# Optimization experiments

Measured on AMD Instinct MI355X. Metric: run time of the kernel, lower is better.

Reference implementation:

```python
import jax, jax.numpy as jnp
import numpy as np

B, L, D, H = 2, 2048, 512, 8
HD = D // H
DIL, WIN, CAUSAL = 2, 256, True
HIDDEN = 4 * D
EPS = 1e-5


def _layer_norm(x, w, b):
    m = jnp.mean(x, axis=-1, keepdims=True)
    v = jnp.mean(jnp.square(x - m), axis=-1, keepdims=True)
    return (x - m) * jax.lax.rsqrt(v + EPS) * w + b


def setup_inputs() -> dict:
    key = jax.random.key(0)
    ks = jax.random.split(key, 6)
    sc = 0.02
    return {
        "x": jax.random.normal(ks[0], (B, L, D), jnp.float32),
        "norm1_w": jnp.ones((D,), jnp.float32),
        "norm1_b": jnp.zeros((D,), jnp.float32),
        "qkv_w": jax.random.normal(ks[1], (3 * D, D), jnp.float32) * sc,
        "qkv_b": jnp.zeros((3 * D,), jnp.float32),
        "out_w": jax.random.normal(ks[2], (D, D), jnp.float32) * sc,
        "out_b": jnp.zeros((D,), jnp.float32),
        "norm2_w": jnp.ones((D,), jnp.float32),
        "norm2_b": jnp.zeros((D,), jnp.float32),
        "ffn_w1": jax.random.normal(ks[3], (HIDDEN, D), jnp.float32) * sc,
        "ffn_b1": jnp.zeros((HIDDEN,), jnp.float32),
        "ffn_w2": jax.random.normal(ks[4], (D, HIDDEN), jnp.float32) * sc,
        "ffn_b2": jnp.zeros((D,), jnp.float32),
    }


def reference(x, norm1_w, norm1_b, qkv_w, qkv_b, out_w, out_b,
              norm2_w, norm2_b, ffn_w1, ffn_b1, ffn_w2, ffn_b2):
    # pre-norm attention block
    h = _layer_norm(x, norm1_w, norm1_b)                       # [B,L,D]
    qkv = h @ qkv_w.T + qkv_b                                  # [B,L,3D]
    q, k, v = jnp.split(qkv, 3, axis=-1)

    def heads(t):  # [B,L,D] -> [B,H,L,HD]
        return t.reshape(B, L, H, HD).transpose(0, 2, 1, 3)

    q, k, v = heads(q), heads(k), heads(v)

    # dilated / windowed / causal keep mask (True = attend)
    idx = jnp.arange(L)
    delta = idx[:, None] - idx[None, :]                        # [L,L]
    keep = (delta % DIL) == 0
    keep &= jnp.abs(delta) <= WIN
    if CAUSAL:
        keep &= delta >= 0

    scale = 1.0 / np.sqrt(HD)
    scores = jnp.einsum('bhqd,bhkd->bhqk', q, k) * scale       # [B,H,L,L]
    scores = jnp.where(keep, scores, jnp.finfo(scores.dtype).min)
    attn = jax.nn.softmax(scores, axis=-1)
    o = jnp.einsum('bhqk,bhkd->bhqd', attn, v)                 # [B,H,L,HD]
    o = o.transpose(0, 2, 1, 3).reshape(B, L, D)
    o = o @ out_w.T + out_b

    x = x + o                                                  # residual (dropout p=0)

    # pre-norm FFN block
    h2 = _layer_norm(x, norm2_w, norm2_b)
    f = jax.nn.gelu(h2 @ ffn_w1.T + ffn_b1, approximate=False)
    f = f @ ffn_w2.T + ffn_b2
    return x + f
```

## Files before the change

kernel.cpp:

```cpp
#include <hip/hip_runtime.h>
#include <stdint.h>

typedef float f32x4 __attribute__((ext_vector_type(4)));
typedef unsigned short u16x4 __attribute__((ext_vector_type(4)));
typedef unsigned short u16x8 __attribute__((ext_vector_type(8)));
typedef __bf16 bf16x8 __attribute__((ext_vector_type(8)));

__device__ __forceinline__ unsigned short f2bf(float f) {
  unsigned u = __float_as_uint(f);
  u += 0x7fffu + ((u >> 16) & 1u);
  return (unsigned short)(u >> 16);
}
__device__ __forceinline__ float bf2f(unsigned short h) {
  return __uint_as_float(((unsigned)h) << 16);
}
__device__ __forceinline__ f32x4 mfma16x16x32(u16x8 a, u16x8 b, f32x4 c) {
  return __builtin_amdgcn_mfma_f32_16x16x32_bf16(
      __builtin_bit_cast(bf16x8, a), __builtin_bit_cast(bf16x8, b), c, 0, 0, 0);
}
__device__ __forceinline__ void gload_lds16(const unsigned short* g, unsigned short* l) {
  __builtin_amdgcn_global_load_lds((__attribute__((address_space(1))) void*)(g),
                                   (__attribute__((address_space(3))) void*)(l), 16, 0, 0);
}
__device__ __forceinline__ int xcd_swz(int bid, int nb) {
  int cpx = nb >> 3;
  return (bid & 7) * cpx + (bid >> 3);
}
__device__ __forceinline__ float gelu_f(float v) {
  float z = 0.7978845608f * (v + 0.044715f * v * v * v);
  float t = __expf(-2.0f * z);
  return v * (1.0f / (1.0f + t));
}

__global__ __launch_bounds__(256)
void prep(const float* __restrict__ wq, unsigned short* __restrict__ dst,
          const float* __restrict__ x, const float* __restrict__ nw,
          const float* __restrict__ nb, unsigned short* __restrict__ hout,
          unsigned short* __restrict__ xbf) {
  if (blockIdx.x < 768) {
    int e = (blockIdx.x * 256 + threadIdx.x) << 2;
    f32x4 v = *(const f32x4*)(wq + e);
    u16x4 o;
    #pragma unroll
    for (int i = 0; i < 4; ++i) o[i] = f2bf(v[i]);
    *(u16x4*)(dst + e) = o;
  } else {
    const int row = ((blockIdx.x - 768) << 2) + (threadIdx.x >> 6);
    const int lane = threadIdx.x & 63;
    const float* xr = x + (size_t)row * 512 + (lane << 3);
    f32x4 v0 = *(const f32x4*)xr;
    f32x4 v1 = *(const f32x4*)(xr + 4);
    float s = 0.f, s2 = 0.f;
    #pragma unroll
    for (int i = 0; i < 4; ++i) { s += v0[i] + v1[i]; s2 += v0[i]*v0[i] + v1[i]*v1[i]; }
    #pragma unroll
    for (int m = 1; m < 64; m <<= 1) { s += __shfl_xor(s, m); s2 += __shfl_xor(s2, m); }
    float mean = s * (1.0f / 512.0f);
    float var  = s2 * (1.0f / 512.0f) - mean * mean;
    float rs = rsqrtf(var + 1e-5f);
    const int d = lane << 3;
    u16x8 o, xo;
    #pragma unroll
    for (int i = 0; i < 8; ++i) {
      float xv = (i < 4) ? v0[i] : v1[i - 4];
      xo[i] = f2bf(xv);
      o[i] = f2bf((xv - mean) * rs * nw[d + i] + nb[d + i]);
    }
    *(u16x8*)(hout + (size_t)row * 512 + d) = o;
    *(u16x8*)(xbf  + (size_t)row * 512 + d) = xo;
  }
}

__global__ __launch_bounds__(256)
void ln_bf16b(const unsigned short* __restrict__ x, const float* __restrict__ w,
              const float* __restrict__ b, unsigned short* __restrict__ out) {
  const int row = (blockIdx.x << 2) + (threadIdx.x >> 6);
  const int lane = threadIdx.x & 63;
  u16x8 xv = *(const u16x8*)(x + (size_t)row * 512 + (lane << 3));
  float f[8];
  float s = 0.f, s2 = 0.f;
  #pragma unroll
  for (int i = 0; i < 8; ++i) { f[i] = bf2f(xv[i]); s += f[i]; s2 += f[i]*f[i]; }
  #pragma unroll
  for (int m = 1; m < 64; m <<= 1) { s += __shfl_xor(s, m); s2 += __shfl_xor(s2, m); }
  float mean = s * (1.0f / 512.0f);
  float var  = s2 * (1.0f / 512.0f) - mean * mean;
  float rs = rsqrtf(var + 1e-5f);
  const int d = lane << 3;
  u16x8 o;
  #pragma unroll
  for (int i = 0; i < 8; ++i)
    o[i] = f2bf((f[i] - mean) * rs * w[d + i] + b[d + i]);
  *(u16x8*)(out + (size_t)row * 512 + d) = o;
}

template<int BM, int BN, int BK, int EPI, int WRV>
__global__ __launch_bounds__(256)
void gemm_bt(const unsigned short* __restrict__ A, const unsigned short* __restrict__ B,
             const float* __restrict__ bias,
             const unsigned short* __restrict__ residB,
             float* __restrict__ Cf, unsigned short* __restrict__ Cb,
             unsigned short* __restrict__ vt,
             int M, int N, int K) {
  constexpr int AM = BM / 32, AN = BN / 32;
  constexpr int CPR = BK / 8;
  constexpr int RPI = 2048 / BK;
  constexpr int LA = BM / RPI, LB = BN / RPI;
  constexpr int XM = (CPR - 1) < 7 ? (CPR - 1) : 7;
  __shared__ __align__(16) unsigned short lA[BM * BK];
  __shared__ __align__(16) unsigned short lB[BN * BK];
  const int tid = threadIdx.x;
  const int wave = tid >> 6, lane = tid & 63;
  const int bid = xcd_swz(blockIdx.x, gridDim.x);
  const int gn = N / BN;
  const int tm = bid / gn, tn = bid - tm * gn;
  const int m0 = tm * BM, n0 = tn * BN;
  const int wr = wave >> 1, wc = wave & 1;
  const int lr = lane & 15;
  const int lk = (lane >> 4) << 3;
  const int rit  = tid / CPR;
  const int csw  = ((tid % CPR) ^ (rit & XM)) << 3;
  f32x4 acc[AM][AN] = {};
  for (int k0 = 0; k0 < K; k0 += BK) {
    #pragma unroll
    for (int it = 0; it < LA; ++it)
      gload_lds16(A + (size_t)(m0 + it * RPI + rit) * K + k0 + csw,
                  &lA[((it << 8) + (wave << 6)) << 3]);
    #pragma unroll
    for (int it = 0; it < LB; ++it)
      gload_lds16(B + (size_t)(n0 + it * RPI + rit) * K + k0 + csw,
                  &lB[((it << 8) + (wave << 6)) << 3]);
    __syncthreads();
    #pragma unroll
    for (int kk = 0; kk < BK; kk += 32) {
      u16x8 af[AM], bfv[AN];
      #pragma unroll
      for (int m = 0; m < AM; ++m) {
        int row = wr * (BM / 2) + (m << 4) + lr;
        int sc = ((((kk + lk) >> 3) ^ (lr & XM)) << 3);
        af[m] = *(const u16x8*)&lA[row * BK + sc];
      }
      #pragma unroll
      for (int n = 0; n < AN; ++n) {
        int row = wc * (BN / 2) + (n << 4) + lr;
        int sc = ((((kk + lk) >> 3) ^ (lr & XM)) << 3);
        bfv[n] = *(const u16x8*)&lB[row * BK + sc];
      }
      #pragma unroll
      for (int m = 0; m < AM; ++m)
        #pragma unroll
        for (int n = 0; n < AN; ++n)
          acc[m][n] = mfma16x16x32(af[m], bfv[n], acc[m][n]);
    }
    __syncthreads();
  }
  const int rbase = m0 + wr * (BM / 2) + ((lane >> 4) << 2);
  const int cbase = n0 + wc * (BN / 2) + lr;
  #pragma unroll
  for (int m = 0; m < AM; ++m) {
    #pragma unroll
    for (int n = 0; n < AN; ++n) {
      int col = cbase + (n << 4);
      float bcol = bias[col];
      #pragma unroll
      for (int i = 0; i < 4; ++i) {
        int row = rbase + (m << 4) + i;
        float v = acc[m][n][i] + bcol;
        size_t off = (size_t)row * N + col;
        if (WRV && col >= 1024) {
          int hh = (col - 1024) >> 6, dd = (col - 1024) & 63;
          int bb = row >> 11, tok = row & 2047;
          long long vrow = ((((((long long)bb << 1) + (tok & 1)) << 3) + hh) << 6) + dd;
          vt[(vrow << 10) + (tok >> 1)] = f2bf(v);
        } else if (EPI == 0) {
          Cb[off] = f2bf(v);
        } else if (EPI == 2) {
          Cb[off] = f2bf(gelu_f(v));
        } else if (EPI == 5) {
          Cb[off] = f2bf(v + bf2f(residB[off]));
        } else {
          Cf[off] = v + bf2f(residB[off]);
        }
      }
    }
  }
}

__global__ __launch_bounds__(256)
void attn_mfma(const unsigned short* __restrict__ qkv,
               const unsigned short* __restrict__ vt,
               unsigned short* __restrict__ out,
               const float* __restrict__ wo, const float* __restrict__ w1,
               const float* __restrict__ w2, unsigned short* __restrict__ wdst) {
  if (blockIdx.x >= 512) {
    int e = ((blockIdx.x - 512) * 256 + threadIdx.x) << 2;
    const float* src; int off;
    if (e < 262144)        { src = wo; off = 0; }
    else if (e < 1310720)  { src = w1; off = 262144; }
    else                   { src = w2; off = 1310720; }
    f32x4 v = *(const f32x4*)(src + e - off);
    u16x4 o;
    #pragma unroll
    for (int i = 0; i < 4; ++i) o[i] = f2bf(v[i]);
    *(u16x4*)(wdst + 786432 + e) = o;
    return;
  }
  __shared__ __align__(16) unsigned short Pl[4][16 * 168];
  const int bid = xcd_swz(blockIdx.x, 512);
  const int qt  = bid & 15;
  const int par = (bid >> 4) & 1;
  const int h   = (bid >> 5) & 7;
  const int b   = bid >> 8;
  const int q0  = qt << 6;
  const int tid = threadIdx.x, wave = tid >> 6, lane = tid & 63;

  const int col = lane & 15;
  const int rg  = lane >> 4;
  const int qt0 = q0 + (wave << 4);
  unsigned short* Pw = Pl[wave];

  const long long qrow = (long long)((b << 11) + ((qt0 + col) << 1) + par);
  const unsigned short* qp = qkv + qrow * 1536 + (h << 6) + (rg << 3);
  u16x8 qa0 = *(const u16x8*)(qp);
  u16x8 qa1 = *(const u16x8*)(qp + 32);

  f32x4 sc[9];
  #pragma unroll
  for (int j = 0; j < 9; ++j) sc[j] = (f32x4){0.f, 0.f, 0.f, 0.f};
  #pragma unroll
  for (int j = 0; j < 9; ++j) {
    int kpj = qt0 - 128 + (j << 4) + col;
    long long krow = (long long)((b << 11) + (kpj << 1) + par);
    const unsigned short* kp = qkv + krow * 1536 + 512 + (h << 6) + (rg << 3);
    u16x8 k0 = *(const u16x8*)(kp);
    u16x8 k1 = *(const u16x8*)(kp + 32);
    sc[j] = mfma16x16x32(qa0, k0, sc[j]);
    sc[j] = mfma16x16x32(qa1, k1, sc[j]);
  }

  const long long vbase = ((long long)((((b << 1) + par) << 3) + h)) << 16;
  u16x8 vb[5][4];
  #pragma unroll
  for (int ks = 0; ks < 5; ++ks) {
    long long kp0 = (long long)qt0 - 128 + (ks << 5) + (rg << 3);
    #pragma unroll
    for (int n = 0; n < 4; ++n)
      vb[ks][n] = *(const u16x8*)(vt + vbase + (((long long)((n << 4) + col)) << 10) + kp0);
  }

  float mrow[4] = {-3e38f, -3e38f, -3e38f, -3e38f};
  #pragma unroll
  for (int j = 0; j < 9; ++j) {
    #pragma unroll
    for (int i = 0; i < 4; ++i) {
      int qr = (rg << 2) + i;
      int jk = (j << 4) + col;
      bool ok = (jk >= qr) && (jk <= qr + 128) && (qt0 + jk >= 128);
      float s = ok ? sc[j][i] * 0.125f : -1e30f;
      sc[j][i] = s;
      mrow[i] = fmaxf(mrow[i], s);
    }
  }
  #pragma unroll
  for (int i = 0; i < 4; ++i)
    #pragma unroll
    for (int m = 1; m < 16; m <<= 1) mrow[i] = fmaxf(mrow[i], __shfl_xor(mrow[i], m));

  float lrow[4] = {0.f, 0.f, 0.f, 0.f};
  #pragma unroll
  for (int j = 0; j < 9; ++j) {
    #pragma unroll
    for (int i = 0; i < 4; ++i) {
      float p = __expf(sc[j][i] - mrow[i]);
      lrow[i] += p;
      Pw[((rg << 2) + i) * 168 + (j << 4) + col] = f2bf(p);
    }
  }
  #pragma unroll
  for (int i = 0; i < 4; ++i)
    Pw[((rg << 2) + i) * 168 + 144 + col] = 0;
  #pragma unroll
  for (int i = 0; i < 4; ++i)
    #pragma unroll
    for (int m = 1; m < 16; m <<= 1) lrow[i] += __shfl_xor(lrow[i], m);
  float inv[4];
  #pragma unroll
  for (int i = 0; i < 4; ++i) inv[i] = 1.0f / lrow[i];

  f32x4 oacc[4] = {};
  #pragma unroll
  for (int ks = 0; ks < 5; ++ks) {
    u16x8 pa = *(const u16x8*)&Pw[col * 168 + (ks << 5) + (rg << 3)];
    #pragma unroll
    for (int n = 0; n < 4; ++n)
      oacc[n] = mfma16x16x32(pa, vb[ks][n], oacc[n]);
  }

  #pragma unroll
  for (int n = 0; n < 4; ++n) {
    #pragma unroll
    for (int i = 0; i < 4; ++i) {
      int q = qt0 + (rg << 2) + i;
      size_t off = ((size_t)((b << 11) + (q << 1) + par)) * 512 + (h << 6) + (n << 4) + col;
      out[off] = f2bf(oacc[n][i] * inv[i]);
    }
  }
}

extern "C" void kernel_launch(void* const* d_in, const int* in_sizes, int n_in,
                              void* d_out, int out_size, void* d_ws, size_t ws_size,
                              hipStream_t stream) {
  const float* x     = (const float*)d_in[0];
  const float* n1w   = (const float*)d_in[1];
  const float* n1b   = (const float*)d_in[2];
  const float* qkv_w = (const float*)d_in[3];
  const float* qkv_b = (const float*)d_in[4];
  const float* out_w = (const float*)d_in[5];
  const float* out_b = (const float*)d_in[6];
  const float* n2w   = (const float*)d_in[7];
  const float* n2b   = (const float*)d_in[8];
  const float* w1    = (const float*)d_in[9];
  const float* b1    = (const float*)d_in[10];
  const float* w2    = (const float*)d_in[11];
  const float* b2    = (const float*)d_in[12];

  char* ws = (char*)d_ws;
  unsigned short* wbf   = (unsigned short*)(ws);
  unsigned short* wq_bf = wbf;
  unsigned short* wo_bf = (unsigned short*)(ws + 1572864);
  unsigned short* w1_bf = (unsigned short*)(ws + 2097152);
  unsigned short* w2_bf = (unsigned short*)(ws + 4194304);
  unsigned short* h_bf  = (unsigned short*)(ws + 6291456);
  unsigned short* qkvb  = (unsigned short*)(ws + 10485760);
  unsigned short* ao_bf = (unsigned short*)(ws + 23068672);
  unsigned short* x1r   = (unsigned short*)(ws + 27262976);
  unsigned short* f1_bf = (unsigned short*)(ws + 10485760);
  unsigned short* vt    = (unsigned short*)(ws + 35651584);
  unsigned short* xbf   = (unsigned short*)(ws + 44040192);
  float* outp = (float*)d_out;

  prep<<<1792, 256, 0, stream>>>(qkv_w, wbf, x, n1w, n1b, h_bf, xbf);
  gemm_bt<128, 64, 128, 0, 1><<<32 * 24, 256, 0, stream>>>(
      h_bf, wq_bf, qkv_b, nullptr, nullptr, qkvb, vt, 4096, 1536, 512);
  attn_mfma<<<512 + 2304, 256, 0, stream>>>(qkvb, vt, ao_bf, out_w, w1, w2, wbf);
  gemm_bt<64, 64, 256, 5, 0><<<64 * 8, 256, 0, stream>>>(
      ao_bf, wo_bf, out_b, xbf, nullptr, x1r, nullptr, 4096, 512, 512);
  ln_bf16b<<<1024, 256, 0, stream>>>(x1r, n2w, n2b, h_bf);
  gemm_bt<128, 128, 128, 2, 0><<<32 * 16, 256, 0, stream>>>(
      h_bf, w1_bf, b1, nullptr, nullptr, f1_bf, nullptr, 4096, 2048, 512);
  gemm_bt<64, 64, 256, 4, 0><<<64 * 8, 256, 0, stream>>>(
      f1_bf, w2_bf, b2, x1r, outp, nullptr, nullptr, 4096, 512, 2048);
}
```

Measured before the change: 84.00 us.

## Fuse LayerNorm and weight conversion into QKV and FFN1 GEMM prologues

Removes the separate prep and LayerNorm-2 kernels. The QKV GEMM now computes row statistics itself, normalizes fp32 x on the fly, and converts fp32 qkv weights to bf16 while staging them into LDS. The FFN1 GEMM normalizes x1 inside its A-tile load. The out-projection residual now reads fp32 x directly instead of a bf16 copy. This drops two launches and several intermediate buffers, but each tile recomputes row stats and the weight conversion, loads go through registers instead of async LDS loads, and K-tiles shrink to 64.

```diff
diff --git a/kernel.cpp b/kernel.cpp
--- a/kernel.cpp
+++ b/kernel.cpp
@@ -33,74 +33,216 @@
 }
 
 __global__ __launch_bounds__(256)
-void prep(const float* __restrict__ wq, unsigned short* __restrict__ dst,
-          const float* __restrict__ x, const float* __restrict__ nw,
-          const float* __restrict__ nb, unsigned short* __restrict__ hout,
-          unsigned short* __restrict__ xbf) {
-  if (blockIdx.x < 768) {
-    int e = (blockIdx.x * 256 + threadIdx.x) << 2;
-    f32x4 v = *(const f32x4*)(wq + e);
-    u16x4 o;
-    #pragma unroll
-    for (int i = 0; i < 4; ++i) o[i] = f2bf(v[i]);
-    *(u16x4*)(dst + e) = o;
-  } else {
-    const int row = ((blockIdx.x - 768) << 2) + (threadIdx.x >> 6);
-    const int lane = threadIdx.x & 63;
-    const float* xr = x + (size_t)row * 512 + (lane << 3);
-    f32x4 v0 = *(const f32x4*)xr;
-    f32x4 v1 = *(const f32x4*)(xr + 4);
+void qkv_fused(const float* __restrict__ x, const float* __restrict__ wq,
+               const float* __restrict__ bias,
+               const float* __restrict__ n1w, const float* __restrict__ n1b,
+               unsigned short* __restrict__ qkvb, unsigned short* __restrict__ vt) {
+  __shared__ __align__(16) unsigned short lA[128 * 64];
+  __shared__ __align__(16) unsigned short lB[64 * 64];
+  __shared__ float sm[128], sr[128];
+  const int tid = threadIdx.x, wave = tid >> 6, lane = tid & 63;
+  const int bid = xcd_swz(blockIdx.x, gridDim.x);
+  const int tm = bid / 24, tn = bid - tm * 24;
+  const int m0 = tm << 7, n0 = tn << 6;
+
+  for (int r = wave; r < 128; r += 4) {
+    const float* xr = x + (size_t)(m0 + r) * 512 + (lane << 3);
+    f32x4 a0 = *(const f32x4*)xr, a1 = *(const f32x4*)(xr + 4);
     float s = 0.f, s2 = 0.f;
     #pragma unroll
-    for (int i = 0; i < 4; ++i) { s += v0[i] + v1[i]; s2 += v0[i]*v0[i] + v1[i]*v1[i]; }
+    for (int i = 0; i < 4; ++i) { s += a0[i] + a1[i]; s2 += a0[i]*a0[i] + a1[i]*a1[i]; }
     #pragma unroll
     for (int m = 1; m < 64; m <<= 1) { s += __shfl_xor(s, m); s2 += __shfl_xor(s2, m); }
-    float mean = s * (1.0f / 512.0f);
-    float var  = s2 * (1.0f / 512.0f) - mean * mean;
-    float rs = rsqrtf(var + 1e-5f);
-    const int d = lane << 3;
-    u16x8 o, xo;
-    #pragma unroll
-    for (int i = 0; i < 8; ++i) {
-      float xv = (i < 4) ? v0[i] : v1[i - 4];
-      xo[i] = f2bf(xv);
-      o[i] = f2bf((xv - mean) * rs * nw[d + i] + nb[d + i]);
-    }
-    *(u16x8*)(hout + (size_t)row * 512 + d) = o;
-    *(u16x8*)(xbf  + (size_t)row * 512 + d) = xo;
+    if (lane == 0) {
+      float mu = s * (1.0f / 512.0f);
+      sm[r] = mu;
+      sr[r] = rsqrtf(s2 * (1.0f / 512.0f) - mu * mu + 1e-5f);
+    }
+  }
+  __syncthreads();
+
+  const int ch = tid & 7, rloc = tid >> 3;
+  const int wr = wave >> 1, wc = wave & 1;
+  const int lr = lane & 15, lk = (lane >> 4) << 3;
+  f32x4 acc[4][2] = {};
+  for (int k0 = 0; k0 < 512; k0 += 64) {
+    #pragma unroll
+    for (int it = 0; it < 4; ++it) {
+      int r = (it << 5) + rloc;
+      const float* src = x + (size_t)(m0 + r) * 512 + k0 + (ch << 3);
+      f32x4 v0 = *(const f32x4*)src, v1 = *(const f32x4*)(src + 4);
+      f32x4 w0 = *(const f32x4*)(n1w + k0 + (ch << 3));
+      f32x4 w1 = *(const f32x4*)(n1w + k0 + (ch << 3) + 4);
+      f32x4 b0 = *(const f32x4*)(n1b + k0 + (ch << 3));
+      f32x4 b1 = *(const f32x4*)(n1b + k0 + (ch << 3) + 4);
+      float mu = sm[r], rs = sr[r];
+      u16x8 o;
+      #pragma unroll
+      for (int j = 0; j < 4; ++j) {
+        o[j]     = f2bf((v0[j] - mu) * rs * w0[j] + b0[j]);
+        o[4 + j] = f2bf((v1[j] - mu) * rs * w1[j] + b1[j]);
+      }
+      *(u16x8*)&lA[(r << 6) + ((ch ^ (r & 7)) << 3)] = o;
+    }
+    #pragma unroll
+    for (int it = 0; it < 2; ++it) {
+      int r = (it << 5) + rloc;
+      const float* src = wq + (size_t)(n0 + r) * 512 + k0 + (ch << 3);
+      f32x4 v0 = *(const f32x4*)src, v1 = *(const f32x4*)(src + 4);
+      u16x8 o;
+      #pragma unroll
+      for (int j = 0; j < 4; ++j) { o[j] = f2bf(v0[j]); o[4 + j] = f2bf(v1[j]); }
+      *(u16x8*)&lB[(r << 6) + ((ch ^ (r & 7)) << 3)] = o;
+    }
+    __syncthreads();
+    #pragma unroll
+    for (int kk = 0; kk < 64; kk += 32) {
+      u16x8 af[4], bfv[2];
+      #pragma unroll
+      for (int m = 0; m < 4; ++m) {
+        int row = (wr << 6) + (m << 4) + lr;
+        af[m] = *(const u16x8*)&lA[(row << 6) + ((((kk + lk) >> 3) ^ (lr & 7)) << 3)];
+      }
+      #pragma unroll
+      for (int n = 0; n < 2; ++n) {
+        int row = (wc << 5) + (n << 4) + lr;
+        bfv[n] = *(const u16x8*)&lB[(row << 6) + ((((kk + lk) >> 3) ^ (lr & 7)) << 3)];
+      }
+      #pragma unroll
+      for (int m = 0; m < 4; ++m)
+        #pragma unroll
+        for (int n = 0; n < 2; ++n)
+          acc[m][n] = mfma16x16x32(af[m], bfv[n], acc[m][n]);
+    }
+    __syncthreads();
+  }
+  const int rbase = m0 + (wr << 6) + ((lane >> 4) << 2);
+  const int cbase = n0 + (wc << 5) + lr;
+  #pragma unroll
+  for (int m = 0; m < 4; ++m) {
+    #pragma unroll
+    for (int n = 0; n < 2; ++n) {
+      int col = cbase + (n << 4);
+      float bcol = bias[col];
+      #pragma unroll
+      for (int i = 0; i < 4; ++i) {
+        int row = rbase + (m << 4) + i;
+        float v = acc[m][n][i] + bcol;
+        if (col >= 1024) {
+          int hh = (col - 1024) >> 6, dd = (col - 1024) & 63;
+          int bb = row >> 11, tok = row & 2047;
+          long long vrow = ((((((long long)bb << 1) + (tok & 1)) << 3) + hh) << 6) + dd;
+          vt[(vrow << 10) + (tok >> 1)] = f2bf(v);
+        } else {
+          qkvb[(size_t)row * 1536 + col] = f2bf(v);
+        }
+      }
+    }
   }
 }
 
 __global__ __launch_bounds__(256)
-void ln_bf16b(const unsigned short* __restrict__ x, const float* __restrict__ w,
-              const float* __restrict__ b, unsigned short* __restrict__ out) {
-  const int row = (blockIdx.x << 2) + (threadIdx.x >> 6);
-  const int lane = threadIdx.x & 63;
-  u16x8 xv = *(const u16x8*)(x + (size_t)row * 512 + (lane << 3));
-  float f[8];
-  float s = 0.f, s2 = 0.f;
-  #pragma unroll
-  for (int i = 0; i < 8; ++i) { f[i] = bf2f(xv[i]); s += f[i]; s2 += f[i]*f[i]; }
-  #pragma unroll
-  for (int m = 1; m < 64; m <<= 1) { s += __shfl_xor(s, m); s2 += __shfl_xor(s2, m); }
-  float mean = s * (1.0f / 512.0f);
-  float var  = s2 * (1.0f / 512.0f) - mean * mean;
-  float rs = rsqrtf(var + 1e-5f);
-  const int d = lane << 3;
-  u16x8 o;
-  #pragma unroll
-  for (int i = 0; i < 8; ++i)
-    o[i] = f2bf((f[i] - mean) * rs * w[d + i] + b[d + i]);
-  *(u16x8*)(out + (size_t)row * 512 + d) = o;
-}
-
-template<int BM, int BN, int BK, int EPI, int WRV>
+void ffn1_fused(const unsigned short* __restrict__ x1r, const unsigned short* __restrict__ B,
+                const float* __restrict__ bias,
+                const float* __restrict__ n2w, const float* __restrict__ n2b,
+                unsigned short* __restrict__ out) {
+  __shared__ __align__(16) unsigned short lA[128 * 64];
+  __shared__ __align__(16) unsigned short lB[128 * 64];
+  __shared__ float sm[128], sr[128];
+  const int tid = threadIdx.x, wave = tid >> 6, lane = tid & 63;
+  const int bid = xcd_swz(blockIdx.x, gridDim.x);
+  const int tm = bid >> 4, tn = bid & 15;
+  const int m0 = tm << 7, n0 = tn << 7;
+
+  for (int r = wave; r < 128; r += 4) {
+    u16x8 xv = *(const u16x8*)(x1r + (size_t)(m0 + r) * 512 + (lane << 3));
+    float s = 0.f, s2 = 0.f;
+    #pragma unroll
+    for (int i = 0; i < 8; ++i) { float f = bf2f(xv[i]); s += f; s2 += f * f; }
+    #pragma unroll
+    for (int m = 1; m < 64; m <<= 1) { s += __shfl_xor(s, m); s2 += __shfl_xor(s2, m); }
+    if (lane == 0) {
+      float mu = s * (1.0f / 512.0f);
+      sm[r] = mu;
+      sr[r] = rsqrtf(s2 * (1.0f / 512.0f) - mu * mu + 1e-5f);
+    }
+  }
+  __syncthreads();
+
+  const int ch = tid & 7, rloc = tid >> 3;
+  const int rit = tid >> 3;
+  const int csw = ((tid & 7) ^ (rit & 7)) << 3;
+  const int wr = wave >> 1, wc = wave & 1;
+  const int lr = lane & 15, lk = (lane >> 4) << 3;
+  f32x4 acc[4][4] = {};
+  for (int k0 = 0; k0 < 512; k0 += 64) {
+    #pragma unroll
+    for (int it = 0; it < 4; ++it) {
+      int r = (it << 5) + rloc;
+      u16x8 xv = *(const u16x8*)(x1r + (size_t)(m0 + r) * 512 + k0 + (ch << 3));
+      f32x4 w0 = *(const f32x4*)(n2w + k0 + (ch << 3));
+      f32x4 w1 = *(const f32x4*)(n2w + k0 + (ch << 3) + 4);
+      f32x4 b0 = *(const f32x4*)(n2b + k0 + (ch << 3));
+      f32x4 b1 = *(const f32x4*)(n2b + k0 + (ch << 3) + 4);
+      float mu = sm[r], rs = sr[r];
+      u16x8 o;
+      #pragma unroll
+      for (int j = 0; j < 4; ++j) {
+        o[j]     = f2bf((bf2f(xv[j])     - mu) * rs * w0[j] + b0[j]);
+        o[4 + j] = f2bf((bf2f(xv[4 + j]) - mu) * rs * w1[j] + b1[j]);
+      }
+      *(u16x8*)&lA[(r << 6) + ((ch ^ (r & 7)) << 3)] = o;
+    }
+    #pragma unroll
+    for (int it = 0; it < 4; ++it)
+      gload_lds16(B + (size_t)(n0 + (it << 5) + rit) * 512 + k0 + csw,
+                  &lB[((it << 8) + (wave << 6)) << 3]);
+    __syncthreads();
+    #pragma unroll
+    for (int kk = 0; kk < 64; kk += 32) {
+      u16x8 af[4], bfv[4];
+      #pragma unroll
+      for (int m = 0; m < 4; ++m) {
+        int row = (wr << 6) + (m << 4) + lr;
+        af[m] = *(const u16x8*)&lA[(row << 6) + ((((kk + lk) >> 3) ^ (lr & 7)) << 3)];
+      }
+      #pragma unroll
+      for (int n = 0; n < 4; ++n) {
+        int row = (wc << 6) + (n << 4) + lr;
+        bfv[n] = *(const u16x8*)&lB[(row << 6) + ((((kk + lk) >> 3) ^ (lr & 7)) << 3)];
+      }
+      #pragma unroll
+      for (int m = 0; m < 4; ++m)
+        #pragma unroll
+        for (int n = 0; n < 4; ++n)
+          acc[m][n] = mfma16x16x32(af[m], bfv[n], acc[m][n]);
+    }
+    __syncthreads();
+  }
+  const int rbase = m0 + (wr << 6) + ((lane >> 4) << 2);
+  const int cbase = n0 + (wc << 6) + lr;
+  #pragma unroll
+  for (int m = 0; m < 4; ++m) {
+    #pragma unroll
+    for (int n = 0; n < 4; ++n) {
+      int col = cbase + (n << 4);
+      float bcol = bias[col];
+      #pragma unroll
+      for (int i = 0; i < 4; ++i) {
+        int row = rbase + (m << 4) + i;
+        float v = acc[m][n][i] + bcol;
+        out[(size_t)row * 2048 + col] = f2bf(gelu_f(v));
+      }
+    }
+  }
+}
+
+template<int BM, int BN, int BK, int EPI>
 __global__ __launch_bounds__(256)
 void gemm_bt(const unsigned short* __restrict__ A, const unsigned short* __restrict__ B,
-             const float* __restrict__ bias,
+             const float* __restrict__ bias, const float* __restrict__ residF,
              const unsigned short* __restrict__ residB,
              float* __restrict__ Cf, unsigned short* __restrict__ Cb,
-             unsigned short* __restrict__ vt,
              int M, int N, int K) {
   constexpr int AM = BM / 32, AN = BN / 32;
   constexpr int CPR = BK / 8;
@@ -118,8 +260,8 @@
   const int wr = wave >> 1, wc = wave & 1;
   const int lr = lane & 15;
   const int lk = (lane >> 4) << 3;
-  const int rit  = tid / CPR;
-  const int csw  = ((tid % CPR) ^ (rit & XM)) << 3;
+  const int rit = tid / CPR;
+  const int csw = ((tid % CPR) ^ (rit & XM)) << 3;
   f32x4 acc[AM][AN] = {};
   for (int k0 = 0; k0 < K; k0 += BK) {
     #pragma unroll
@@ -167,17 +309,8 @@
         int row = rbase + (m << 4) + i;
         float v = acc[m][n][i] + bcol;
         size_t off = (size_t)row * N + col;
-        if (WRV && col >= 1024) {
-          int hh = (col - 1024) >> 6, dd = (col - 1024) & 63;
-          int bb = row >> 11, tok = row & 2047;
-          long long vrow = ((((((long long)bb << 1) + (tok & 1)) << 3) + hh) << 6) + dd;
-          vt[(vrow << 10) + (tok >> 1)] = f2bf(v);
-        } else if (EPI == 0) {
-          Cb[off] = f2bf(v);
-        } else if (EPI == 2) {
-          Cb[off] = f2bf(gelu_f(v));
-        } else if (EPI == 5) {
-          Cb[off] = f2bf(v + bf2f(residB[off]));
+        if (EPI == 3) {
+          Cb[off] = f2bf(v + residF[off]);
         } else {
           Cf[off] = v + bf2f(residB[off]);
         }
@@ -326,28 +459,21 @@
 
   char* ws = (char*)d_ws;
   unsigned short* wbf   = (unsigned short*)(ws);
-  unsigned short* wq_bf = wbf;
   unsigned short* wo_bf = (unsigned short*)(ws + 1572864);
   unsigned short* w1_bf = (unsigned short*)(ws + 2097152);
   unsigned short* w2_bf = (unsigned short*)(ws + 4194304);
-  unsigned short* h_bf  = (unsigned short*)(ws + 6291456);
   unsigned short* qkvb  = (unsigned short*)(ws + 10485760);
   unsigned short* ao_bf = (unsigned short*)(ws + 23068672);
   unsigned short* x1r   = (unsigned short*)(ws + 27262976);
   unsigned short* f1_bf = (unsigned short*)(ws + 10485760);
   unsigned short* vt    = (unsigned short*)(ws + 35651584);
-  unsigned short* xbf   = (unsigned short*)(ws + 44040192);
   float* outp = (float*)d_out;
 
-  prep<<<1792, 256, 0, stream>>>(qkv_w, wbf, x, n1w, n1b, h_bf, xbf);
-  gemm_bt<128, 64, 128, 0, 1><<<32 * 24, 256, 0, stream>>>(
-      h_bf, wq_bf, qkv_b, nullptr, nullptr, qkvb, vt, 4096, 1536, 512);
+  qkv_fused<<<768, 256, 0, stream>>>(x, qkv_w, qkv_b, n1w, n1b, qkvb, vt);
   attn_mfma<<<512 + 2304, 256, 0, stream>>>(qkvb, vt, ao_bf, out_w, w1, w2, wbf);
-  gemm_bt<64, 64, 256, 5, 0><<<64 * 8, 256, 0, stream>>>(
-      ao_bf, wo_bf, out_b, xbf, nullptr, x1r, nullptr, 4096, 512, 512);
-  ln_bf16b<<<1024, 256, 0, stream>>>(x1r, n2w, n2b, h_bf);
-  gemm_bt<128, 128, 128, 2, 0><<<32 * 16, 256, 0, stream>>>(
-      h_bf, w1_bf, b1, nullptr, nullptr, f1_bf, nullptr, 4096, 2048, 512);
-  gemm_bt<64, 64, 256, 4, 0><<<64 * 8, 256, 0, stream>>>(
-      f1_bf, w2_bf, b2, x1r, outp, nullptr, nullptr, 4096, 512, 2048);
-}
+  gemm_bt<64, 64, 256, 3><<<64 * 8, 256, 0, stream>>>(
+      ao_bf, wo_bf, out_b, x, nullptr, nullptr, x1r, 4096, 512, 512);
+  ffn1_fused<<<512, 256, 0, stream>>>(x1r, w1_bf, b1, n2w, n2b, f1_bf);
+  gemm_bt<64, 64, 256, 4><<<64 * 8, 256, 0, stream>>>(
+      f1_bf, w2_bf, b2, nullptr, x1r, outp, nullptr, 4096, 512, 2048);
+}
```

Measured after the change: 129.5 us. 1.54x slower.

## Split attention key range across wave pairs with LDS softmax merge

Applied to the files above, without the earlier changes.

Each attention block now covers 32 queries instead of 64, and pairs of waves split the 144-key window into two halves (80 and 64 keys). Each wave computes a partial max, sum and output, then the partials are merged through shared memory with a flash-style rescale before the bf16 store. This doubles the block count and shortens the per-wave dependency chain to improve latency hiding and occupancy. In exchange it adds a __syncthreads, extra LDS traffic and merge arithmetic, loads Q twice per block, and loads V inside the loop instead of prefetching it.

```diff
diff --git a/kernel.cpp b/kernel.cpp
--- a/kernel.cpp
+++ b/kernel.cpp
@@ -187,13 +187,13 @@
 }
 
 __global__ __launch_bounds__(256)
-void attn_mfma(const unsigned short* __restrict__ qkv,
-               const unsigned short* __restrict__ vt,
-               unsigned short* __restrict__ out,
-               const float* __restrict__ wo, const float* __restrict__ w1,
-               const float* __restrict__ w2, unsigned short* __restrict__ wdst) {
-  if (blockIdx.x >= 512) {
-    int e = ((blockIdx.x - 512) * 256 + threadIdx.x) << 2;
+void attn_split(const unsigned short* __restrict__ qkv,
+                const unsigned short* __restrict__ vt,
+                unsigned short* __restrict__ out,
+                const float* __restrict__ wo, const float* __restrict__ w1,
+                const float* __restrict__ w2, unsigned short* __restrict__ wdst) {
+  if (blockIdx.x >= 1024) {
+    int e = ((blockIdx.x - 1024) * 256 + threadIdx.x) << 2;
     const float* src; int off;
     if (e < 262144)        { src = wo; off = 0; }
     else if (e < 1310720)  { src = w1; off = 262144; }
@@ -205,18 +205,22 @@
     *(u16x4*)(wdst + 786432 + e) = o;
     return;
   }
-  __shared__ __align__(16) unsigned short Pl[4][16 * 168];
-  const int bid = xcd_swz(blockIdx.x, 512);
-  const int qt  = bid & 15;
-  const int par = (bid >> 4) & 1;
-  const int h   = (bid >> 5) & 7;
-  const int b   = bid >> 8;
-  const int q0  = qt << 6;
+  __shared__ __align__(16) unsigned short Pl[4][16 * 104];
+  __shared__ float Olds[4][16 * 68];
+  __shared__ float Mm[2][2][16], Ll[2][2][16];
+  const int bid = xcd_swz(blockIdx.x, 1024);
+  const int qt5 = bid & 31;
+  const int par = (bid >> 5) & 1;
+  const int h   = (bid >> 6) & 7;
+  const int b   = bid >> 9;
+  const int q0  = qt5 << 5;
   const int tid = threadIdx.x, wave = tid >> 6, lane = tid & 63;
 
   const int col = lane & 15;
   const int rg  = lane >> 4;
-  const int qt0 = q0 + (wave << 4);
+  const int qtile = wave & 1, kh = wave >> 1;
+  const int qt0 = q0 + (qtile << 4);
+  const int NJ = kh ? 4 : 5, JB = kh ? 5 : 0;
   unsigned short* Pw = Pl[wave];
 
   const long long qrow = (long long)((b << 11) + ((qt0 + col) << 1) + par);
@@ -224,12 +228,12 @@
   u16x8 qa0 = *(const u16x8*)(qp);
   u16x8 qa1 = *(const u16x8*)(qp + 32);
 
-  f32x4 sc[9];
-  #pragma unroll
-  for (int j = 0; j < 9; ++j) sc[j] = (f32x4){0.f, 0.f, 0.f, 0.f};
-  #pragma unroll
-  for (int j = 0; j < 9; ++j) {
-    int kpj = qt0 - 128 + (j << 4) + col;
+  f32x4 sc[5];
+  #pragma unroll
+  for (int j = 0; j < 5; ++j) sc[j] = (f32x4){0.f, 0.f, 0.f, 0.f};
+  for (int j = 0; j < NJ; ++j) {
+    int jj = JB + j;
+    int kpj = qt0 - 128 + (jj << 4) + col;
     long long krow = (long long)((b << 11) + (kpj << 1) + par);
     const unsigned short* kp = qkv + krow * 1536 + 512 + (h << 6) + (rg << 3);
     u16x8 k0 = *(const u16x8*)(kp);
@@ -238,23 +242,12 @@
     sc[j] = mfma16x16x32(qa1, k1, sc[j]);
   }
 
-  const long long vbase = ((long long)((((b << 1) + par) << 3) + h)) << 16;
-  u16x8 vb[5][4];
-  #pragma unroll
-  for (int ks = 0; ks < 5; ++ks) {
-    long long kp0 = (long long)qt0 - 128 + (ks << 5) + (rg << 3);
-    #pragma unroll
-    for (int n = 0; n < 4; ++n)
-      vb[ks][n] = *(const u16x8*)(vt + vbase + (((long long)((n << 4) + col)) << 10) + kp0);
-  }
-
-  float mrow[4] = {-3e38f, -3e38f, -3e38f, -3e38f};
-  #pragma unroll
-  for (int j = 0; j < 9; ++j) {
+  float mrow[4] = {-1e30f, -1e30f, -1e30f, -1e30f};
+  for (int j = 0; j < NJ; ++j) {
     #pragma unroll
     for (int i = 0; i < 4; ++i) {
       int qr = (rg << 2) + i;
-      int jk = (j << 4) + col;
+      int jk = ((JB + j) << 4) + col;
       bool ok = (jk >= qr) && (jk <= qr + 128) && (qt0 + jk >= 128);
       float s = ok ? sc[j][i] * 0.125f : -1e30f;
       sc[j][i] = s;
@@ -267,43 +260,68 @@
     for (int m = 1; m < 16; m <<= 1) mrow[i] = fmaxf(mrow[i], __shfl_xor(mrow[i], m));
 
   float lrow[4] = {0.f, 0.f, 0.f, 0.f};
-  #pragma unroll
-  for (int j = 0; j < 9; ++j) {
+  for (int j = 0; j < NJ; ++j) {
     #pragma unroll
     for (int i = 0; i < 4; ++i) {
       float p = __expf(sc[j][i] - mrow[i]);
       lrow[i] += p;
-      Pw[((rg << 2) + i) * 168 + (j << 4) + col] = f2bf(p);
-    }
+      Pw[((rg << 2) + i) * 104 + (j << 4) + col] = f2bf(p);
+    }
+  }
+  if (!kh) {
+    #pragma unroll
+    for (int i = 0; i < 4; ++i)
+      Pw[((rg << 2) + i) * 104 + 80 + col] = 0;
   }
   #pragma unroll
   for (int i = 0; i < 4; ++i)
-    Pw[((rg << 2) + i) * 168 + 144 + col] = 0;
-  #pragma unroll
-  for (int i = 0; i < 4; ++i)
     #pragma unroll
     for (int m = 1; m < 16; m <<= 1) lrow[i] += __shfl_xor(lrow[i], m);
-  float inv[4];
-  #pragma unroll
-  for (int i = 0; i < 4; ++i) inv[i] = 1.0f / lrow[i];
-
+
+  const long long vbase = ((long long)((((b << 1) + par) << 3) + h)) << 16;
   f32x4 oacc[4] = {};
-  #pragma unroll
-  for (int ks = 0; ks < 5; ++ks) {
-    u16x8 pa = *(const u16x8*)&Pw[col * 168 + (ks << 5) + (rg << 3)];
-    #pragma unroll
-    for (int n = 0; n < 4; ++n)
-      oacc[n] = mfma16x16x32(pa, vb[ks][n], oacc[n]);
-  }
-
-  #pragma unroll
-  for (int n = 0; n < 4; ++n) {
+  const int KSTEPS = kh ? 2 : 3;
+  for (int ks = 0; ks < KSTEPS; ++ks) {
+    int kk = ks << 5;
+    u16x8 pa = *(const u16x8*)&Pw[col * 104 + kk + (rg << 3)];
+    long long kp0 = (long long)qt0 - 128 + (JB << 4) + kk + (rg << 3);
+    #pragma unroll
+    for (int n = 0; n < 4; ++n) {
+      u16x8 vbv = *(const u16x8*)(vt + vbase + (((long long)((n << 4) + col)) << 10) + kp0);
+      oacc[n] = mfma16x16x32(pa, vbv, oacc[n]);
+    }
+  }
+
+  const int obuf = (qtile << 1) + kh;
+  #pragma unroll
+  for (int n = 0; n < 4; ++n)
+    #pragma unroll
+    for (int i = 0; i < 4; ++i)
+      Olds[obuf][((rg << 2) + i) * 68 + (n << 4) + col] = oacc[n][i];
+  if (col == 0) {
     #pragma unroll
     for (int i = 0; i < 4; ++i) {
-      int q = qt0 + (rg << 2) + i;
-      size_t off = ((size_t)((b << 11) + (q << 1) + par)) * 512 + (h << 6) + (n << 4) + col;
-      out[off] = f2bf(oacc[n][i] * inv[i]);
-    }
+      Mm[qtile][kh][(rg << 2) + i] = mrow[i];
+      Ll[qtile][kh][(rg << 2) + i] = lrow[i];
+    }
+  }
+  __syncthreads();
+
+  const int dcol = (kh << 5) + (lane & 31);
+  const int rb = (lane >> 5) << 3;
+  #pragma unroll
+  for (int r8 = 0; r8 < 8; ++r8) {
+    int row = rb + r8;
+    float mA = Mm[qtile][0][row], mB = Mm[qtile][1][row];
+    float lA = Ll[qtile][0][row], lB = Ll[qtile][1][row];
+    float m = fmaxf(mA, mB);
+    float fA = __expf(mA - m), fB = __expf(mB - m);
+    float oa = Olds[(qtile << 1)][row * 68 + dcol];
+    float ob = Olds[(qtile << 1) + 1][row * 68 + dcol];
+    float val = (oa * fA + ob * fB) / (lA * fA + lB * fB);
+    int q = q0 + (qtile << 4) + row;
+    size_t off = ((size_t)((b << 11) + (q << 1) + par)) * 512 + (h << 6) + dcol;
+    out[off] = f2bf(val);
   }
 }
 
@@ -342,7 +360,7 @@
   prep<<<1792, 256, 0, stream>>>(qkv_w, wbf, x, n1w, n1b, h_bf, xbf);
   gemm_bt<128, 64, 128, 0, 1><<<32 * 24, 256, 0, stream>>>(
       h_bf, wq_bf, qkv_b, nullptr, nullptr, qkvb, vt, 4096, 1536, 512);
-  attn_mfma<<<512 + 2304, 256, 0, stream>>>(qkvb, vt, ao_bf, out_w, w1, w2, wbf);
+  attn_split<<<1024 + 2304, 256, 0, stream>>>(qkvb, vt, ao_bf, out_w, w1, w2, wbf);
   gemm_bt<64, 64, 256, 5, 0><<<64 * 8, 256, 0, stream>>>(
       ao_bf, wo_bf, out_b, xbf, nullptr, x1r, nullptr, 4096, 512, 512);
   ln_bf16b<<<1024, 256, 0, stream>>>(x1r, n2w, n2b, h_bf);
```

Result: slower. 85.75 us (+2.1%).
